# Kernel tuning notes

Hardware: AMD Instinct MI355X
Metric: run time of the kernel (lower is better)

The kernel has to match this reference:

```python
import jax, jax.numpy as jnp
import numpy as np

EPS = 1e-5

def _layernorm(x, g, b):
    m = jnp.mean(x, axis=-1, keepdims=True)
    v = jnp.mean(jnp.square(x - m), axis=-1, keepdims=True)
    return (x - m) * jax.lax.rsqrt(v + EPS) * g + b

def setup_inputs() -> dict:
    key = jax.random.key(0)
    ks = jax.random.split(key, 4)
    B, N, D = 8, 256, 128
    h = jax.random.normal(ks[0], (B, N, D), dtype=jnp.float32)
    adj_J = jax.random.normal(ks[1], (B, N, N), dtype=jnp.float32)
    W_msg = jax.random.normal(ks[2], (D, 2 * D + 1), dtype=jnp.float32) * 0.05
    W_upd = jax.random.normal(ks[3], (D, 2 * D), dtype=jnp.float32) * 0.05
    return {
        "h": h, "adj_J": adj_J,
        "W_msg": W_msg, "b_msg": jnp.zeros((D,), jnp.float32),
        "g_msg": jnp.ones((D,), jnp.float32), "beta_msg": jnp.zeros((D,), jnp.float32),
        "W_upd": W_upd, "b_upd": jnp.zeros((D,), jnp.float32),
        "g_upd": jnp.ones((D,), jnp.float32), "beta_upd": jnp.zeros((D,), jnp.float32),
    }

def reference(h, adj_J, W_msg, b_msg, g_msg, beta_msg, W_upd, b_upd, g_upd, beta_upd):
    B, N, D = h.shape
    # Split msg Linear weight: cat([h_target, h_source, J]) @ W.T is separable.
    Wt = W_msg[:, :D]        # acts on h_target (node i, dim 1)
    Ws = W_msg[:, D:2 * D]   # acts on h_source (node j, dim 2)
    wJ = W_msg[:, 2 * D]     # acts on scalar J
    # pre[b,i,j,e] = h[b,i]@Wt.T + h[b,j]@Ws.T + J[b,i,j]*wJ + b
    pre = (jnp.einsum('bid,ed->bie', h, Wt)[:, :, None, :]
           + jnp.einsum('bjd,ed->bje', h, Ws)[:, None, :, :]
           + adj_J[..., None] * wJ
           + b_msg)
    messages = jax.nn.silu(_layernorm(pre, g_msg, beta_msg))  # (B,N,N,D)
    # mask out self-messages (j == i) then sum over sources j
    idx = jnp.arange(N)
    agg = jnp.sum(messages, axis=2) - messages[:, idx, idx, :]  # (B,N,D)
    upd_pre = (jnp.einsum('bnd,ed->bne', h, W_upd[:, :D])
               + jnp.einsum('bnd,ed->bne', agg, W_upd[:, D:])
               + b_upd)
    dh = jax.nn.silu(_layernorm(upd_pre, g_upd, beta_upd))
    return h + dh
```

## Files before the change

### kernel.cpp

```cpp
#include <hip/hip_runtime.h>

#define BB 8
#define NN 256
#define DD 128
#define SW 257
#define SU 256
#define EPSV 1e-5f

__device__ __forceinline__ float wave_reduce_add(float v) {
#pragma unroll
  for (int off = 32; off > 0; off >>= 1) v += __shfl_xor(v, off, 64);
  return v;
}

__global__ __launch_bounds__(256) void k_proj(
    const float* __restrict__ h, const float* __restrict__ Wm,
    const float* __restrict__ bmsg, const float* __restrict__ Wu,
    float* __restrict__ u, float* __restrict__ s,
    float* __restrict__ rowA, float* __restrict__ rowB,
    float* __restrict__ rowD2, float* __restrict__ rowE2,
    float* __restrict__ wtilv, float* __restrict__ wut) {
  const int blk = blockIdx.x;
  const int b = blk >> 6;
  const int r0 = (blk & 63) * 4;
  const int tid = threadIdx.x;
  const int half = tid >> 7, e = tid & 127;
  const int wv = tid >> 6, lane = tid & 63;

  __shared__ float hs[4][DD];
  __shared__ float pS[4][4], pw[2], pQ[4][4], pD[4][4];

  const float* hb = h + (size_t)(b * NN + r0) * DD;
  if (tid < DD) {
#pragma unroll
    for (int r = 0; r < 4; ++r) hs[r][e] = hb[r * DD + e];
  }
  if (tid >= DD && tid < DD + 64) {
    const int i = blk * 64 + (tid - DD);
    const int d = i >> 7, e2 = i & 127;
    wut[i] = Wu[(size_t)e2 * SU + d];
  }
  __syncthreads();

  float acc[4];
  const float bm = (half == 0) ? bmsg[e] : 0.f;
#pragma unroll
  for (int r = 0; r < 4; ++r) acc[r] = bm;

  const float* wr = Wm + (size_t)e * SW + half * DD;
#pragma unroll 8
  for (int k = 0; k < DD; k += 4) {
    const float4 w4 = *(const float4*)(wr + k);
#pragma unroll
    for (int r = 0; r < 4; ++r) {
      const float4 hv = *(const float4*)(&hs[r][k]);
      acc[r] = fmaf(hv.x, w4.x, acc[r]);
      acc[r] = fmaf(hv.y, w4.y, acc[r]);
      acc[r] = fmaf(hv.z, w4.z, acc[r]);
      acc[r] = fmaf(hv.w, w4.w, acc[r]);
    }
  }

  const float we = Wm[(size_t)e * SW + 2 * DD];
#pragma unroll
  for (int r = 0; r < 4; ++r) {
    const float sm = wave_reduce_add(acc[r]);
    if (lane == 0) pS[wv][r] = sm;
  }
  {
    const float sw = wave_reduce_add(we);
    if (lane == 0 && wv < 2) pw[wv] = sw;
  }
  __syncthreads();

  const int b2 = half * 2;
  const float muw = (pw[0] + pw[1]) * (1.f / DD);
  const float wtil = we - muw;
  float c[4];
#pragma unroll
  for (int r = 0; r < 4; ++r)
    c[r] = acc[r] - (pS[b2][r] + pS[b2 + 1][r]) * (1.f / DD);

  float* outp = (half == 0 ? u : s) + (size_t)(b * NN + r0) * DD;
#pragma unroll
  for (int r = 0; r < 4; ++r) outp[r * DD + e] = c[r];
  if (blk == 0 && half == 0) wtilv[e] = wtil;

#pragma unroll
  for (int r = 0; r < 4; ++r) {
    const float q = wave_reduce_add(c[r] * c[r]);
    const float dd = wave_reduce_add(c[r] * wtil);
    if (lane == 0) { pQ[wv][r] = q; pD[wv][r] = dd; }
  }
  __syncthreads();
  if (tid < 4) {
    const int row = b * NN + r0 + tid;
    rowA[row]  = pQ[0][tid] + pQ[1][tid];
    rowD2[row] = 2.f * (pD[0][tid] + pD[1][tid]);
    rowB[row]  = pQ[2][tid] + pQ[3][tid];
    rowE2[row] = 2.f * (pD[2][tid] + pD[3][tid]);
  }
}

__global__ __launch_bounds__(256) void k_msgf1(
    const float* __restrict__ h, const float* __restrict__ u,
    const float* __restrict__ s, const float* __restrict__ adj,
    const float* __restrict__ rowA, const float* __restrict__ rowB,
    const float* __restrict__ rowD2, const float* __restrict__ rowE2,
    const float* __restrict__ wtilv, const float* __restrict__ g,
    const float* __restrict__ be, const float* __restrict__ wut,
    const float* __restrict__ bu, const float* __restrict__ gu,
    const float* __restrict__ beu, float* __restrict__ out) {
  const int blk = blockIdx.x;
  const int b = blk >> 8, i = blk & 255;
  const int tid = threadIdx.x, lane = tid & 63, wv = tid >> 6;
  const int bNN = b * NN;

  __shared__ __align__(16) float st_[32 * 132];
  __shared__ __align__(16) float urow_[DD];
  __shared__ __align__(16) float hrow_[DD];
  __shared__ float2 pak[32];
  __shared__ float pm[2], pq[2];

  if (tid < DD)       urow_[tid] = u[(size_t)blk * DD + tid];
  else                hrow_[tid - DD] = h[(size_t)blk * DD + (tid - DD)];
  const float2 wt2 = *(const float2*)(wtilv + 2 * lane);
  const float2 g2  = *(const float2*)(g + 2 * lane);
  const float2 be2 = *(const float2*)(be + 2 * lane);
  const float C = wave_reduce_add(fmaf(wt2.x, wt2.x, wt2.y * wt2.y));
  const float Ai = rowA[blk];
  const float D2i = rowD2[blk];
  __syncthreads();
  const float2 uu = *(const float2*)(&urow_[2 * lane]);

  float acc0 = 0.f, acc1 = 0.f;
  const float* sb = s + (size_t)bNN * DD;
  const float* adjrow = adj + (size_t)blk * NN;

  for (int tile = 0; tile < 8; ++tile) {
    const int t0 = tile * 32;
    __syncthreads();
    {
      const int r = tid >> 5, c4 = (tid & 31) * 4;
#pragma unroll
      for (int p = 0; p < 4; ++p) {
        const int row = p * 8 + r;
        *(float4*)(&st_[row * 132 + c4]) =
            *(const float4*)(sb + (size_t)(t0 + row) * DD + c4);
      }
    }
    __syncthreads();
    {
      const int j = tid >> 3, seg = tid & 7, k0 = seg * 16;
      float d0 = 0.f;
#pragma unroll
      for (int k = 0; k < 16; k += 4) {
        const float4 sv = *(const float4*)(&st_[j * 132 + k0 + k]);
        const float4 uv = *(const float4*)(&urow_[k0 + k]);
        d0 = fmaf(sv.x, uv.x, d0); d0 = fmaf(sv.y, uv.y, d0);
        d0 = fmaf(sv.z, uv.z, d0); d0 = fmaf(sv.w, uv.w, d0);
      }
#pragma unroll
      for (int m = 1; m < 8; m <<= 1) d0 += __shfl_xor(d0, m, 64);
      if (seg == 0) {
        const int jg = t0 + j;
        const float Bj = rowB[bNN + jg], E2j = rowE2[bNN + jg];
        const float a0 = adjrow[jg];
        const float q0 = fmaf(a0, fmaf(a0, C, D2i + E2j), Ai + Bj + 2.f * d0);
        pak[j] = make_float2(a0, __builtin_amdgcn_rsqf(fmaf(q0, 1.f / DD, EPSV)));
      }
    }
    __syncthreads();
    for (int jj = wv; jj < 32; jj += 4) {
      const int jg = t0 + jj;
      if (jg == i) continue;
      const float2 ss = *(const float2*)(&st_[jj * 132 + 2 * lane]);
      const float2 p = pak[jj];
      const float x0 = fmaf(p.x, wt2.x, uu.x + ss.x);
      const float x1 = fmaf(p.x, wt2.y, uu.y + ss.y);
      const float y0 = fmaf(x0 * p.y, g2.x, be2.x);
      const float y1 = fmaf(x1 * p.y, g2.y, be2.y);
      acc0 = fmaf(y0, __builtin_amdgcn_rcpf(1.f + __expf(-y0)), acc0);
      acc1 = fmaf(y1, __builtin_amdgcn_rcpf(1.f + __expf(-y1)), acc1);
    }
  }

  __syncthreads();
  *(float2*)(&st_[wv * DD + 2 * lane]) = make_float2(acc0, acc1);
  __syncthreads();
  if (tid < DD) {
    st_[4 * DD + tid] = st_[0 * DD + tid] + st_[1 * DD + tid] +
                        st_[2 * DD + tid] + st_[3 * DD + tid];
  }
  __syncthreads();

  const int half = tid >> 7, e = tid & 127;
  float v = (half == 0) ? bu[e] : 0.f;
  {
    const float* xin = (half == 0) ? hrow_ : &st_[4 * DD];
    const float* wcol = wut + (size_t)half * DD * DD + e;
#pragma unroll 8
    for (int k = 0; k < DD; ++k) v = fmaf(xin[k], wcol[(size_t)k * DD], v);
  }
  if (half == 1) urow_[e] = v;
  __syncthreads();
  if (half == 0) {
    v += urow_[e];
    const float sm = wave_reduce_add(v), sq = wave_reduce_add(v * v);
    if (lane == 0) { pm[wv] = sm; pq[wv] = sq; }
  }
  __syncthreads();
  if (half == 0) {
    const float mean = (pm[0] + pm[1]) * (1.f / DD);
    const float var = (pq[0] + pq[1]) * (1.f / DD) - mean * mean;
    const float rs = __builtin_amdgcn_rsqf(var + EPSV);
    const float y = fmaf((v - mean) * rs, gu[e], beu[e]);
    const float sg = __builtin_amdgcn_rcpf(1.f + __expf(-y));
    out[(size_t)blk * DD + e] = hrow_[e] + y * sg;
  }
}

extern "C" void kernel_launch(void* const* d_in, const int* in_sizes, int n_in,
                              void* d_out, int out_size, void* d_ws, size_t ws_size,
                              hipStream_t stream) {
  const float* h    = (const float*)d_in[0];
  const float* adj  = (const float*)d_in[1];
  const float* Wm   = (const float*)d_in[2];
  const float* bmsg = (const float*)d_in[3];
  const float* gmsg = (const float*)d_in[4];
  const float* bemsg= (const float*)d_in[5];
  const float* Wu   = (const float*)d_in[6];
  const float* bupd = (const float*)d_in[7];
  const float* gupd = (const float*)d_in[8];
  const float* beupd= (const float*)d_in[9];
  float* out = (float*)d_out;

  float* ws    = (float*)d_ws;
  float* u     = ws;
  float* s     = u + BB * NN * DD;
  float* rowA  = s + BB * NN * DD;
  float* rowB  = rowA + BB * NN;
  float* rowD2 = rowB + BB * NN;
  float* rowE2 = rowD2 + BB * NN;
  float* wtilv = rowE2 + BB * NN;
  float* wut   = wtilv + DD;

  k_proj<<<512, 256, 0, stream>>>(h, Wm, bmsg, Wu, u, s, rowA, rowB, rowD2,
                                  rowE2, wtilv, wut);
  k_msgf1<<<2048, 256, 0, stream>>>(h, u, s, adj, rowA, rowB, rowD2, rowE2,
                                    wtilv, gmsg, bemsg, wut, bupd, gupd,
                                    beupd, out);
}
```

Measured before the change: 62.47 us.

## Rework message kernel to register-prefetch source tiles and drop per-tile LDS syncs

The message-aggregation kernel no longer stages 32-row source tiles in shared memory behind three barriers per tile. Each wave now owns 8 source rows per tile, double-buffers them in registers with prefetch of the next tile, and broadcasts the per-row rsqrt and adjacency values with readlane. The adjacency and row statistics are preloaded once into LDS. The SiLU math is folded into the log2 domain with packed float2 ops and a single shared reciprocal for two lanes. This raises register pressure and reads global memory directly with less coalescing, in exchange for removing the barriers and LDS traffic.

Result: no change. 62.80 us (+0.5%).

```diff
diff --git a/kernel.cpp b/kernel.cpp
--- a/kernel.cpp
+++ b/kernel.cpp
@@ -6,11 +6,19 @@
 #define SW 257
 #define SU 256
 #define EPSV 1e-5f
+#define LOG2E 1.4426950408889634f
+#define LN2F 0.6931471805599453f
+
+typedef float v2f __attribute__((ext_vector_type(2)));
 
 __device__ __forceinline__ float wave_reduce_add(float v) {
 #pragma unroll
   for (int off = 32; off > 0; off >>= 1) v += __shfl_xor(v, off, 64);
   return v;
+}
+
+__device__ __forceinline__ float readlane_f(float v, int l) {
+  return __uint_as_float(__builtin_amdgcn_readlane(__float_as_uint(v), l));
 }
 
 __global__ __launch_bounds__(256) void k_proj(
@@ -102,7 +110,7 @@
   }
 }
 
-__global__ __launch_bounds__(256) void k_msgf1(
+__global__ __launch_bounds__(256) void k_msgr1(
     const float* __restrict__ h, const float* __restrict__ u,
     const float* __restrict__ s, const float* __restrict__ adj,
     const float* __restrict__ rowA, const float* __restrict__ rowB,
@@ -114,99 +122,122 @@
   const int blk = blockIdx.x;
   const int b = blk >> 8, i = blk & 255;
   const int tid = threadIdx.x, lane = tid & 63, wv = tid >> 6;
+  const int seg = lane & 7, jloc = lane >> 3;
+  const int jrow = wv * 8 + jloc;
   const int bNN = b * NN;
 
-  __shared__ __align__(16) float st_[32 * 132];
   __shared__ __align__(16) float urow_[DD];
   __shared__ __align__(16) float hrow_[DD];
-  __shared__ float2 pak[32];
+  __shared__ __align__(16) float4 pakr_[NN];
+  __shared__ __align__(16) float sacc_[5 * DD];
   __shared__ float pm[2], pq[2];
 
   if (tid < DD)       urow_[tid] = u[(size_t)blk * DD + tid];
   else                hrow_[tid - DD] = h[(size_t)blk * DD + (tid - DD)];
+  pakr_[tid] = make_float4(adj[(size_t)blk * NN + tid],
+                           rowB[bNN + tid], rowE2[bNN + tid], 0.f);
   const float2 wt2 = *(const float2*)(wtilv + 2 * lane);
   const float2 g2  = *(const float2*)(g + 2 * lane);
   const float2 be2 = *(const float2*)(be + 2 * lane);
+  const v2f wt2v  = {wt2.x, wt2.y};
+  const v2f gl2v  = {g2.x * LOG2E, g2.y * LOG2E};
+  const v2f bel2v = {be2.x * LOG2E, be2.y * LOG2E};
   const float C = wave_reduce_add(fmaf(wt2.x, wt2.x, wt2.y * wt2.y));
   const float Ai = rowA[blk];
   const float D2i = rowD2[blk];
   __syncthreads();
+
   const float2 uu = *(const float2*)(&urow_[2 * lane]);
-
-  float acc0 = 0.f, acc1 = 0.f;
-  const float* sb = s + (size_t)bNN * DD;
-  const float* adjrow = adj + (size_t)blk * NN;
-
-  for (int tile = 0; tile < 8; ++tile) {
-    const int t0 = tile * 32;
-    __syncthreads();
-    {
-      const int r = tid >> 5, c4 = (tid & 31) * 4;
-#pragma unroll
-      for (int p = 0; p < 4; ++p) {
-        const int row = p * 8 + r;
-        *(float4*)(&st_[row * 132 + c4]) =
-            *(const float4*)(sb + (size_t)(t0 + row) * DD + c4);
+  const v2f uu0v = {uu.x, uu.y};
+  float4 ua[4];
+#pragma unroll
+  for (int c = 0; c < 4; ++c)
+    ua[c] = *(const float4*)(&urow_[seg * 16 + c * 4]);
+
+  const float* cA_ptr = s + (size_t)(bNN + wv * 8) * DD + 2 * lane;
+  const float* sB_ptr = s + (size_t)(bNN + jrow) * DD + seg * 16;
+
+  float2 colreg[2][8];
+  float4 sreg[4];
+#pragma unroll
+  for (int k = 0; k < 8; ++k)
+    colreg[0][k] = *(const float2*)(cA_ptr + (size_t)k * DD);
+#pragma unroll
+  for (int c = 0; c < 4; ++c)
+    sreg[c] = *(const float4*)(sB_ptr + c * 4);
+
+  v2f accA = {0.f, 0.f};
+
+#pragma unroll
+  for (int t = 0; t < 8; ++t) {
+    float d0 = 0.f;
+#pragma unroll
+    for (int c = 0; c < 4; ++c) {
+      d0 = fmaf(sreg[c].x, ua[c].x, d0); d0 = fmaf(sreg[c].y, ua[c].y, d0);
+      d0 = fmaf(sreg[c].z, ua[c].z, d0); d0 = fmaf(sreg[c].w, ua[c].w, d0);
+    }
+    d0 += __shfl_xor(d0, 1, 64);
+    d0 += __shfl_xor(d0, 2, 64);
+    d0 += __shfl_xor(d0, 4, 64);
+
+    const int jgq = t * 32 + jrow;
+    const float4 pk = pakr_[jgq];
+    const float q0 = fmaf(pk.x, fmaf(pk.x, C, D2i + pk.z), Ai + pk.y + 2.f * d0);
+    const float rs0v = __builtin_amdgcn_rsqf(fmaf(q0, 1.f / DD, EPSV));
+    const float a0v = pk.x;
+
+    if (t < 7) {
+#pragma unroll
+      for (int c = 0; c < 4; ++c)
+        sreg[c] = *(const float4*)(sB_ptr + (size_t)(t + 1) * 32 * DD + c * 4);
+#pragma unroll
+      for (int k = 0; k < 8; ++k)
+        colreg[(t + 1) & 1][k] =
+            *(const float2*)(cA_ptr + (size_t)((t + 1) * 32 + k) * DD);
+    }
+
+#pragma unroll
+    for (int k = 0; k < 8; ++k) {
+      const float rs0k = readlane_f(rs0v, k * 8);
+      const float a0k = readlane_f(a0v, k * 8);
+      const int jgk = t * 32 + wv * 8 + k;
+      if (jgk != i) {
+        const float2 ss = colreg[t & 1][k];
+        const v2f ssv = {ss.x, ss.y};
+        const v2f x = a0k * wt2v + (uu0v + ssv);
+        const v2f rg = rs0k * gl2v;
+        const v2f z = x * rg + bel2v;
+        const float e0 = exp2f(-z.x), e1 = exp2f(-z.y);
+        const float p0 = 1.f + e0, p1 = 1.f + e1;
+        const float r = __builtin_amdgcn_rcpf(p0 * p1);
+        const v2f w = {r * p1, r * p0};
+        accA = z * w + accA;
       }
     }
-    __syncthreads();
-    {
-      const int j = tid >> 3, seg = tid & 7, k0 = seg * 16;
-      float d0 = 0.f;
-#pragma unroll
-      for (int k = 0; k < 16; k += 4) {
-        const float4 sv = *(const float4*)(&st_[j * 132 + k0 + k]);
-        const float4 uv = *(const float4*)(&urow_[k0 + k]);
-        d0 = fmaf(sv.x, uv.x, d0); d0 = fmaf(sv.y, uv.y, d0);
-        d0 = fmaf(sv.z, uv.z, d0); d0 = fmaf(sv.w, uv.w, d0);
-      }
-#pragma unroll
-      for (int m = 1; m < 8; m <<= 1) d0 += __shfl_xor(d0, m, 64);
-      if (seg == 0) {
-        const int jg = t0 + j;
-        const float Bj = rowB[bNN + jg], E2j = rowE2[bNN + jg];
-        const float a0 = adjrow[jg];
-        const float q0 = fmaf(a0, fmaf(a0, C, D2i + E2j), Ai + Bj + 2.f * d0);
-        pak[j] = make_float2(a0, __builtin_amdgcn_rsqf(fmaf(q0, 1.f / DD, EPSV)));
-      }
-    }
-    __syncthreads();
-    for (int jj = wv; jj < 32; jj += 4) {
-      const int jg = t0 + jj;
-      if (jg == i) continue;
-      const float2 ss = *(const float2*)(&st_[jj * 132 + 2 * lane]);
-      const float2 p = pak[jj];
-      const float x0 = fmaf(p.x, wt2.x, uu.x + ss.x);
-      const float x1 = fmaf(p.x, wt2.y, uu.y + ss.y);
-      const float y0 = fmaf(x0 * p.y, g2.x, be2.x);
-      const float y1 = fmaf(x1 * p.y, g2.y, be2.y);
-      acc0 = fmaf(y0, __builtin_amdgcn_rcpf(1.f + __expf(-y0)), acc0);
-      acc1 = fmaf(y1, __builtin_amdgcn_rcpf(1.f + __expf(-y1)), acc1);
-    }
-  }
-
-  __syncthreads();
-  *(float2*)(&st_[wv * DD + 2 * lane]) = make_float2(acc0, acc1);
+  }
+
+  *(float2*)(&sacc_[wv * DD + 2 * lane]) =
+      make_float2(accA.x * LN2F, accA.y * LN2F);
   __syncthreads();
   if (tid < DD) {
-    st_[4 * DD + tid] = st_[0 * DD + tid] + st_[1 * DD + tid] +
-                        st_[2 * DD + tid] + st_[3 * DD + tid];
+    sacc_[4 * DD + tid] = sacc_[0 * DD + tid] + sacc_[1 * DD + tid] +
+                          sacc_[2 * DD + tid] + sacc_[3 * DD + tid];
   }
   __syncthreads();
 
   const int half = tid >> 7, e = tid & 127;
-  float v = (half == 0) ? bu[e] : 0.f;
+  float v0 = (half == 0) ? bu[e] : 0.f;
   {
-    const float* xin = (half == 0) ? hrow_ : &st_[4 * DD];
+    const float* xin = (half == 0) ? hrow_ : &sacc_[4 * DD];
     const float* wcol = wut + (size_t)half * DD * DD + e;
 #pragma unroll 8
-    for (int k = 0; k < DD; ++k) v = fmaf(xin[k], wcol[(size_t)k * DD], v);
-  }
-  if (half == 1) urow_[e] = v;
+    for (int k = 0; k < DD; ++k) v0 = fmaf(xin[k], wcol[(size_t)k * DD], v0);
+  }
+  if (half == 1) urow_[e] = v0;
   __syncthreads();
   if (half == 0) {
-    v += urow_[e];
-    const float sm = wave_reduce_add(v), sq = wave_reduce_add(v * v);
+    v0 += urow_[e];
+    const float sm = wave_reduce_add(v0), sq = wave_reduce_add(v0 * v0);
     if (lane == 0) { pm[wv] = sm; pq[wv] = sq; }
   }
   __syncthreads();
@@ -214,7 +245,7 @@
     const float mean = (pm[0] + pm[1]) * (1.f / DD);
     const float var = (pq[0] + pq[1]) * (1.f / DD) - mean * mean;
     const float rs = __builtin_amdgcn_rsqf(var + EPSV);
-    const float y = fmaf((v - mean) * rs, gu[e], beu[e]);
+    const float y = fmaf((v0 - mean) * rs, gu[e], beu[e]);
     const float sg = __builtin_amdgcn_rcpf(1.f + __expf(-y));
     out[(size_t)blk * DD + e] = hrow_[e] + y * sg;
   }
@@ -247,7 +278,7 @@
 
   k_proj<<<512, 256, 0, stream>>>(h, Wm, bmsg, Wu, u, s, rowA, rowB, rowD2,
                                   rowE2, wtilv, wut);
-  k_msgf1<<<2048, 256, 0, stream>>>(h, u, s, adj, rowA, rowB, rowD2, rowE2,
+  k_msgr1<<<2048, 256, 0, stream>>>(h, u, s, adj, rowA, rowB, rowD2, rowE2,
                                     wtilv, gmsg, bemsg, wut, bupd, gupd,
                                     beupd, out);
 }
```
